# Kernel optimization log

Measured on AMD Instinct MI355X. Metric: run time of the kernel, lower is better.

## Reference

```python
import jax, jax.numpy as jnp
import numpy as np

TAU = 1.5
SCALE = 0.125
EPS = 1e-5
H = 8

@jax.custom_vjp
def spike(u):
    return (u >= 0.0).astype(u.dtype)

def _spike_fwd(u):
    return spike(u), u

def _spike_bwd(u, g):
    # ATan surrogate gradient, alpha=2 (spikingjelly default)
    return (g / (1.0 + (jnp.pi * u) ** 2),)

spike.defvjp(_spike_fwd, _spike_bwd)

def lif_ms(xt):
    # xt: (T, ...) multi-step LIF, decay_input=True, v_th=1, hard reset to 0, detach_reset
    def step(v, x):
        v = v + (x - v) / TAU
        s = spike(v - 1.0)
        v = v * (1.0 - jax.lax.stop_gradient(s))
        return v, s
    _, s = jax.lax.scan(step, jnp.zeros_like(xt[0]), xt)
    return s

def bn(x, g, b, m, var):
    # eval-mode BatchNorm1d over channel dim of (B, C, L)
    inv = g / jnp.sqrt(var + EPS)
    return (x - m[None, :, None]) * inv[None, :, None] + b[None, :, None]

def setup_inputs() -> dict:
    key = jax.random.key(0)
    ks = jax.random.split(key, 16)
    B, C, T, N = 8, 512, 4, 256
    w_scale = 1.0 / np.sqrt(C)
    inp = {
        'x': jax.random.normal(ks[0], (B, C, T, N), jnp.float32),
        'wq': jax.random.normal(ks[1], (C, C), jnp.float32) * w_scale,
        'wk': jax.random.normal(ks[2], (C, C), jnp.float32) * w_scale,
        'wv': jax.random.normal(ks[3], (C, C), jnp.float32) * w_scale,
        'wp': jax.random.normal(ks[4], (C, C), jnp.float32) * w_scale,
        'bp': jnp.zeros((C,), jnp.float32),
        'gq': jax.random.uniform(ks[5], (C,), jnp.float32, 0.5, 1.5),
        'bq': jax.random.uniform(ks[6], (C,), jnp.float32),
        'mq': jnp.zeros((C,), jnp.float32),
        'vq': jnp.ones((C,), jnp.float32),
        'gk': jax.random.uniform(ks[7], (C,), jnp.float32, 0.5, 1.5),
        'bk': jax.random.uniform(ks[8], (C,), jnp.float32),
        'mk': jnp.zeros((C,), jnp.float32),
        'vk': jnp.ones((C,), jnp.float32),
        'gv': jax.random.uniform(ks[9], (C,), jnp.float32, 0.5, 1.5),
        'bv': jax.random.uniform(ks[10], (C,), jnp.float32),
        'mv': jnp.zeros((C,), jnp.float32),
        'vv': jnp.ones((C,), jnp.float32),
        'gp': jax.random.uniform(ks[11], (C,), jnp.float32, 0.5, 1.5),
        'bpn': jax.random.uniform(ks[12], (C,), jnp.float32),
        'mp': jnp.zeros((C,), jnp.float32),
        'vp': jnp.ones((C,), jnp.float32),
    }
    return inp

def reference(x, wq, wk, wv, wp, bp, gq, bq, mq, vq, gk, bk, mk, vk,
              gv, bv, mv, vv, gp, bpn, mp, vp):
    B, C, T, N = x.shape
    L = T * N
    d = C // H

    # proj_bn then multi-step proj_lif over time dim
    xb = bn(x.reshape(B, C, L), gp, bpn, mp, vp).reshape(B, C, T, N)
    s0 = lif_ms(jnp.transpose(xb, (2, 0, 1, 3)))            # (T,B,C,N)
    x_for_qkv = jnp.transpose(s0, (1, 2, 0, 3)).reshape(B, C, L)  # (B,C,L)

    def qkv_branch(w, g, b_, m, v_):
        y = bn(jnp.einsum('oc,bcl->bol', w, x_for_qkv), g, b_, m, v_)
        y = y.reshape(B, C, T, N)
        sy = lif_ms(jnp.transpose(y, (2, 0, 1, 3)))         # (T,B,C,N)
        sy = jnp.transpose(sy, (1, 0, 3, 2)).reshape(B, L, C)  # (B,T,N,C)->(B,L,C)
        return jnp.transpose(sy.reshape(B, L, H, d), (0, 2, 1, 3))  # (B,H,L,d)

    q = qkv_branch(wq, gq, bq, mq, vq)
    k = qkv_branch(wk, gk, bk, mk, vk)
    v = qkv_branch(wv, gv, bv, mv, vv)

    attn = jnp.einsum('bhqd,bhkd->bhqk', q, k)              # no softmax
    o = jnp.einsum('bhqk,bhkd->bhqd', attn, v) * SCALE
    o = jnp.transpose(o, (0, 1, 3, 2)).reshape(B, C, L)

    # single-step attn_lif: v = o/tau from zero state, spike at threshold 1
    s = spike(o / TAU - 1.0)

    out = jnp.einsum('oc,bcl->bol', wp, s) + bp[None, :, None]
    return out.reshape(B, C, T, N)
```

## Files before the change

kernel.cpp:

```cpp
#include <hip/hip_runtime.h>
#include <hip/hip_bf16.h>


#define NB 8
#define NC 512
#define NT 4
#define NN 256
#define NL 1024
#define NH 8
#define ND 64
#define BCL (NB*NC*NL)

typedef __attribute__((ext_vector_type(8))) short  short8v;
typedef __attribute__((ext_vector_type(8))) unsigned short us8;
typedef __attribute__((ext_vector_type(4))) unsigned short us4;
typedef __attribute__((ext_vector_type(4))) float f32x4;

__device__ __forceinline__ float bu2f(unsigned short u) {
  return __uint_as_float(((unsigned)u) << 16);
}
__device__ __forceinline__ unsigned short f2bu(float f) {
  unsigned b = __float_as_uint(f);
  return (unsigned short)((b + 0x7FFFu + ((b >> 16) & 1u)) >> 16);
}

__global__ void k_prep(const float* __restrict__ wq, const float* __restrict__ wk,
                       const float* __restrict__ wv, const float* __restrict__ wp,
                       const float* __restrict__ x,
                       const float* __restrict__ g,  const float* __restrict__ bt,
                       const float* __restrict__ mu, const float* __restrict__ var,
                       unsigned short* __restrict__ H2,
                       unsigned short* __restrict__ ST0) {
  if (blockIdx.x < 512) {
    int gi = blockIdx.x * 256 + threadIdx.x;
    int p = gi >> 15;
    int o = (gi >> 6) & 511;
    int k8 = gi & 63;
    int rt = o >> 7, r = o & 127;
    int k0i = k8 >> 3, chunk = k8 & 7;
    const float* W = (p == 0) ? wq : (p == 1) ? wk : (p == 2) ? wv : wp;
    const float* src = W + (size_t)o * NC + k8 * 8;
    us8 a[3];
#pragma unroll
    for (int i = 0; i < 8; i++) {
      float w = src[i];
      unsigned short u1 = f2bu(w);
      float r1 = w - bu2f(u1);
      unsigned short u2 = f2bu(r1);
      float r2 = r1 - bu2f(u2);
      unsigned short u3 = f2bu(r2);
      a[0][i] = u1; a[1][i] = u2; a[2][i] = u3;
    }
#pragma unroll
    for (int j = 0; j < 3; j++) {
      size_t off = ((size_t)((((p * 3 + j) * 4 + rt) * 8 + k0i) * 8 + chunk)) * 1024
                   + (size_t)r * 8;
      *(us8*)&H2[off] = a[j];
    }
  } else {
    int bidx = blockIdx.x - 512;
    int b  = bidx >> 6;
    int c0 = (bidx & 63) * 8;
    int n  = threadIdx.x;
    unsigned short spk[NT][8];
#pragma unroll
    for (int i = 0; i < 8; i++) {
      int c = c0 + i;
      float inv = g[c] / sqrtf(var[c] + 1e-5f);
      float m = mu[c], be = bt[c];
      const float* xp = x + ((size_t)(b * NC + c)) * NL + n;
      float v = 0.f;
#pragma unroll
      for (int t = 0; t < NT; t++) {
        float y = (xp[t * NN] - m) * inv + be;
        v = v + (y - v) / 1.5f;
        unsigned short s = 0;
        if (v - 1.0f >= 0.f) { s = 0x3F80; v = 0.f; }
        spk[t][i] = s;
      }
    }
#pragma unroll
    for (int t = 0; t < NT; t++) {
      us8 pk;
#pragma unroll
      for (int i = 0; i < 8; i++) pk[i] = spk[t][i];
      *(us8*)&ST0[((size_t)b * NL + t * NN + n) * NC + c0] = pk;
    }
  }
}

__global__ __launch_bounds__(256) void
k_qkv(const unsigned short* __restrict__ H2,
      const unsigned short* __restrict__ ST0,
      const float* __restrict__ gq, const float* __restrict__ bq,
      const float* __restrict__ mq, const float* __restrict__ vq,
      const float* __restrict__ gk, const float* __restrict__ bk,
      const float* __restrict__ mk, const float* __restrict__ vk,
      const float* __restrict__ gv, const float* __restrict__ bv,
      const float* __restrict__ mv, const float* __restrict__ vv,
      unsigned short* __restrict__ STq, unsigned short* __restrict__ STk,
      unsigned short* __restrict__ STv) {
  __shared__ __align__(16) unsigned short sB[2][128 * 64];

  int id = blockIdx.x;
  int xcd = id & 7, slot = id >> 3;
  int qq = xcd * 96 + slot;
  int grp = qq >> 6, mi = qq & 63;
  int p = grp >> 2, rt = grp & 3;
  int b = mi >> 3;
  int n0 = (mi & 7) * 32;

  int tid = threadIdx.x;
  int w = tid >> 6, lane = tid & 63, quad = lane >> 4, l15 = lane & 15;
  int xorv = l15 & 7;

  const unsigned short* Sb = ST0 + (size_t)b * NL * NC;
  const unsigned short* Hbase = H2 + ((size_t)((p * 3) * 4 + rt) * 8) * 8192;

  f32x4 acc[2][8];
#pragma unroll
  for (int ri = 0; ri < 2; ri++)
#pragma unroll
    for (int jj = 0; jj < 8; jj++) acc[ri][jj] = (f32x4){0.f, 0.f, 0.f, 0.f};

  short8v A0[2][3][2], A1[2][3][2];

#define QLOADA(DST, K0I)                                                     \
  _Pragma("unroll") for (int ks = 0; ks < 2; ks++) {                         \
    int c8 = ks * 4 + quad;                                                  \
    _Pragma("unroll") for (int j = 0; j < 3; j++) {                          \
      const unsigned short* Hj =                                             \
          Hbase + ((size_t)(j * 4 * 8 + (K0I))) * 8192 + (size_t)c8 * 1024;  \
      DST[ks][j][0] = *(const short8v*)&Hj[(w * 32 + l15) * 8];              \
      DST[ks][j][1] = *(const short8v*)&Hj[(w * 32 + 16 + l15) * 8];         \
    }                                                                        \
  }

  QLOADA(A0, 0);

  us8 breg[4];
  int ccs[4], segs[4];
  size_t bsrc[4];
#pragma unroll
  for (int i = 0; i < 4; i++) {
    int idx = tid + i * 256;
    int cc = idx >> 3, seg = idx & 7;
    int t = (cc >> 4) & 3, nn = (cc & 15) | ((cc >> 6) << 4);
    ccs[i] = cc; segs[i] = seg;
    bsrc[i] = (size_t)(t * NN + n0 + nn) * NC + seg * 8;
  }
#pragma unroll
  for (int i = 0; i < 4; i++) breg[i] = *(const us8*)&Sb[bsrc[i]];
#pragma unroll
  for (int i = 0; i < 4; i++)
    *(us8*)&sB[0][ccs[i] * 64 + ((segs[i] ^ (ccs[i] & 7)) << 3)] = breg[i];

#define QBPRE(K0N)                                                           \
  _Pragma("unroll") for (int i = 0; i < 4; i++)                              \
    breg[i] = *(const us8*)&Sb[bsrc[i] + (size_t)(K0N) * 64];

#define QBWRITE(BUFN)                                                        \
  _Pragma("unroll") for (int i = 0; i < 4; i++)                              \
    *(us8*)&sB[BUFN][ccs[i] * 64 + ((segs[i] ^ (ccs[i] & 7)) << 3)] = breg[i];

#define QMFMAS(AR, BUF)                                                      \
  _Pragma("unroll") for (int ks = 0; ks < 2; ks++) {                         \
    int c8 = ks * 4 + quad;                                                  \
    int poff = (c8 ^ xorv) << 3;                                             \
    short8v bf[8];                                                           \
    _Pragma("unroll") for (int jj = 0; jj < 8; jj++)                         \
      bf[jj] = *(const short8v*)&sB[BUF][(jj * 16 + l15) * 64 + poff];       \
    _Pragma("unroll") for (int j = 0; j < 3; j++)                            \
      _Pragma("unroll") for (int jj = 0; jj < 8; jj++) {                     \
        acc[0][jj] = __builtin_amdgcn_mfma_f32_16x16x32_bf16(                \
            AR[ks][j][0], bf[jj], acc[0][jj], 0, 0, 0);                      \
        acc[1][jj] = __builtin_amdgcn_mfma_f32_16x16x32_bf16(                \
            AR[ks][j][1], bf[jj], acc[1][jj], 0, 0, 0);                      \
      }                                                                      \
  }

#define QSTEP(K0I, ACUR, ANXT)                                               \
  __syncthreads();                                                           \
  { if ((K0I) < 7) { QLOADA(ANXT, (K0I) + 1); } }                            \
  { if ((K0I) < 7) { QBPRE((K0I) + 1); } }                                   \
  QMFMAS(ACUR, (K0I) & 1);                                                   \
  { if ((K0I) < 7) { QBWRITE(((K0I) & 1) ^ 1); } }

  QSTEP(0, A0, A1)
  QSTEP(1, A1, A0)
  QSTEP(2, A0, A1)
  QSTEP(3, A1, A0)
  QSTEP(4, A0, A1)
  QSTEP(5, A1, A0)
  QSTEP(6, A0, A1)
  QSTEP(7, A1, A0)

#undef QLOADA
#undef QBPRE
#undef QBWRITE
#undef QMFMAS
#undef QSTEP

  const float *g, *bb, *mpt, *vr;
  unsigned short* So;
  if (p == 0)      { g = gq; bb = bq; mpt = mq; vr = vq; So = STq; }
  else if (p == 1) { g = gk; bb = bk; mpt = mk; vr = vk; So = STk; }
  else             { g = gv; bb = bv; mpt = mv; vr = vv; So = STv; }
  So += (size_t)b * NL * NC;

#pragma unroll
  for (int ri = 0; ri < 2; ri++) {
    int ob = rt * 128 + w * 32 + ri * 16 + quad * 4;
    float av[4], mvv[4], bvv[4];
#pragma unroll
    for (int r = 0; r < 4; r++) {
      av[r]  = g[ob + r] / sqrtf(vr[ob + r] + 1e-5f);
      mvv[r] = mpt[ob + r];
      bvv[r] = bb[ob + r];
    }
#pragma unroll
    for (int nh = 0; nh < 2; nh++) {
      int n = n0 + (nh << 4) + l15;
      unsigned short sp[4][4];
#pragma unroll
      for (int r = 0; r < 4; r++) {
        float vmem = 0.f;
#pragma unroll
        for (int t = 0; t < NT; t++) {
          float y = (acc[ri][nh * 4 + t][r] - mvv[r]) * av[r] + bvv[r];
          vmem = vmem + (y - vmem) / 1.5f;
          unsigned short s = 0;
          if (vmem - 1.0f >= 0.f) { s = 0x3F80; vmem = 0.f; }
          sp[t][r] = s;
        }
      }
#pragma unroll
      for (int t = 0; t < NT; t++) {
        us4 pk;
#pragma unroll
        for (int r = 0; r < 4; r++) pk[r] = sp[t][r];
        *(us4*)&So[(size_t)(t * NN + n) * NC + ob] = pk;
      }
    }
  }
}

__global__ void k_kvM(const unsigned short* __restrict__ STk,
                      const unsigned short* __restrict__ STv,
                      float* __restrict__ Mpart) {
  int bh = blockIdx.x, ch = blockIdx.y;
  int b = bh >> 3, h = bh & 7;
  const unsigned short* Kp = STk + (size_t)b * NL * NC + h * ND;
  const unsigned short* Vp = STv + (size_t)b * NL * NC + h * ND;
  __shared__ float sK[64][72];
  __shared__ float sV[64][72];
  int tid = threadIdx.x, tx = tid & 15, ty = tid >> 4;
  float acc[4][4] = {};
  for (int lt = 0; lt < 2; lt++) {
    int lb = ch * 128 + lt * 64;
#pragma unroll
    for (int i = 0; i < 2; i++) {
      int idx = tid + i * 256;
      int r = idx >> 3, seg = idx & 7;
      us8 kv = *(const us8*)&Kp[(size_t)(lb + r) * NC + seg * 8];
      us8 vv = *(const us8*)&Vp[(size_t)(lb + r) * NC + seg * 8];
#pragma unroll
      for (int q2 = 0; q2 < 8; q2++) {
        sK[r][seg * 8 + q2] = bu2f(kv[q2]);
        sV[r][seg * 8 + q2] = bu2f(vv[q2]);
      }
    }
    __syncthreads();
#pragma unroll 8
    for (int lc = 0; lc < 64; lc++) {
      float kvx[4], vvx[4];
#pragma unroll
      for (int i = 0; i < 4; i++) kvx[i] = sK[lc][ty * 4 + i];
#pragma unroll
      for (int j2 = 0; j2 < 4; j2++) vvx[j2] = sV[lc][tx * 4 + j2];
#pragma unroll
      for (int i = 0; i < 4; i++)
#pragma unroll
        for (int j2 = 0; j2 < 4; j2++)
          acc[i][j2] += kvx[i] * vvx[j2];
    }
    __syncthreads();
  }
  float* Mp = Mpart + ((size_t)ch * 64 + bh) * 4096;
#pragma unroll
  for (int i = 0; i < 4; i++) {
    float4 v4 = make_float4(acc[i][0], acc[i][1], acc[i][2], acc[i][3]);
    *(float4*)&Mp[(ty * 4 + i) * ND + tx * 4] = v4;
  }
}

__global__ __launch_bounds__(256) void
k_attn(const unsigned short* __restrict__ STq,
       const float* __restrict__ Mpart,
       unsigned short* __restrict__ STs) {
  __shared__ unsigned short MT1[64 * 64];
  __shared__ unsigned short MT2[64 * 64];
  int lt = blockIdx.x, bh = blockIdx.y;
  int b = bh >> 3, h = bh & 7;
  int tid = threadIdx.x;
  int w = tid >> 6, lane = tid & 63, quad = lane >> 4, l15 = lane & 15;

#pragma unroll
  for (int i = 0; i < 4; i++) {
    int idx4 = tid + i * 256;
    float4 s = ((const float4*)Mpart)[(size_t)bh * 1024 + idx4];
#pragma unroll
    for (int ch = 1; ch < 8; ch++) {
      float4 t = ((const float4*)Mpart)[((size_t)ch * 64 + bh) * 1024 + idx4];
      s.x += t.x; s.y += t.y; s.z += t.z; s.w += t.w;
    }
    int e = idx4 >> 4;
    int dd0 = (idx4 * 4) & 63;
    int chunk = e >> 3;
    float sv[4] = {s.x, s.y, s.z, s.w};
#pragma unroll
    for (int r = 0; r < 4; r++) {
      int dd = dd0 + r;
      unsigned short u1 = f2bu(sv[r]);
      unsigned short u2 = f2bu(sv[r] - bu2f(u1));
      int pos = dd * 64 + (((chunk ^ (dd & 7)) << 3) | (e & 7));
      MT1[pos] = u1;
      MT2[pos] = u2;
    }
  }
  __syncthreads();

  const unsigned short* Qp = STq + (size_t)b * NL * NC + h * ND;
  int lbase = lt * 256 + w * 64;

  f32x4 acc[4][4];
#pragma unroll
  for (int dt = 0; dt < 4; dt++)
#pragma unroll
    for (int j = 0; j < 4; j++) acc[dt][j] = (f32x4){0.f, 0.f, 0.f, 0.f};

#pragma unroll
  for (int ks = 0; ks < 2; ks++) {
    short8v bq[4];
#pragma unroll
    for (int ltile = 0; ltile < 4; ltile++)
      bq[ltile] = *(const short8v*)&Qp[(size_t)(lbase + ltile * 16 + l15) * NC
                                       + ks * 32 + quad * 8];
    int c8 = ks * 4 + quad;
#pragma unroll
    for (int dt = 0; dt < 4; dt++) {
      int dd = dt * 16 + l15;
      int off = dd * 64 + ((c8 ^ (dd & 7)) << 3);
      short8v a1 = *(const short8v*)&MT1[off];
      short8v a2 = *(const short8v*)&MT2[off];
#pragma unroll
      for (int ltile = 0; ltile < 4; ltile++) {
        acc[dt][ltile] = __builtin_amdgcn_mfma_f32_16x16x32_bf16(a1, bq[ltile], acc[dt][ltile], 0, 0, 0);
        acc[dt][ltile] = __builtin_amdgcn_mfma_f32_16x16x32_bf16(a2, bq[ltile], acc[dt][ltile], 0, 0, 0);
      }
    }
  }

  unsigned short* Sp = STs + (size_t)b * NL * NC + h * ND;
#pragma unroll
  for (int dt = 0; dt < 4; dt++)
#pragma unroll
    for (int ltile = 0; ltile < 4; ltile++) {
      int l = lbase + ltile * 16 + l15;
      int dd = dt * 16 + quad * 4;
      us4 pk;
#pragma unroll
      for (int r = 0; r < 4; r++) pk[r] = (acc[dt][ltile][r] >= 12.0f) ? 0x3F80 : 0;
      *(us4*)&Sp[(size_t)l * NC + dd] = pk;
    }
}

__global__ __launch_bounds__(256) void
k_out(const unsigned short* __restrict__ H2,
      const unsigned short* __restrict__ STs,
      const float* __restrict__ bp, float* __restrict__ out) {
  __shared__ __align__(16) unsigned short sB[2][64 * 64];

  int id = blockIdx.x;
  int xcd = id & 7, slot = id >> 3;
  int qq = xcd * 64 + slot;
  int rt = qq >> 7;
  int mi = qq & 127;
  int b  = mi >> 4;
  int l0 = (mi & 15) * 64;

  int tid = threadIdx.x;
  int w = tid >> 6, lane = tid & 63, quad = lane >> 4, l15 = lane & 15;
  int xorv = l15 & 7;

  const unsigned short* Sb = STs + (size_t)b * NL * NC;
  const unsigned short* Hbase = H2 + ((size_t)(9 * 4 + rt) * 8) * 8192;

  f32x4 acc[2][4];
#pragma unroll
  for (int ri = 0; ri < 2; ri++)
#pragma unroll
    for (int jj = 0; jj < 4; jj++) acc[ri][jj] = (f32x4){0.f, 0.f, 0.f, 0.f};

  short8v A0[2][3][2], A1[2][3][2];

#define OLOADA(DST, K0I)                                                     \
  _Pragma("unroll") for (int ks = 0; ks < 2; ks++) {                         \
    int c8 = ks * 4 + quad;                                                  \
    _Pragma("unroll") for (int j = 0; j < 3; j++) {                          \
      const unsigned short* Hj =                                             \
          Hbase + ((size_t)(j * 4 * 8 + (K0I))) * 8192 + (size_t)c8 * 1024;  \
      DST[ks][j][0] = *(const short8v*)&Hj[(w * 32 + l15) * 8];              \
      DST[ks][j][1] = *(const short8v*)&Hj[(w * 32 + 16 + l15) * 8];         \
    }                                                                        \
  }

  OLOADA(A0, 0);

  us8 breg[2];
  int ccs[2], segs[2];
  size_t bsrc[2];
#pragma unroll
  for (int i = 0; i < 2; i++) {
    int idx = tid + i * 256;
    int cc = idx >> 3, seg = idx & 7;
    ccs[i] = cc; segs[i] = seg;
    bsrc[i] = (size_t)(l0 + cc) * NC + seg * 8;
  }
#pragma unroll
  for (int i = 0; i < 2; i++) breg[i] = *(const us8*)&Sb[bsrc[i]];
#pragma unroll
  for (int i = 0; i < 2; i++)
    *(us8*)&sB[0][ccs[i] * 64 + ((segs[i] ^ (ccs[i] & 7)) << 3)] = breg[i];

#define OBPRE(K0N)                                                           \
  _Pragma("unroll") for (int i = 0; i < 2; i++)                              \
    breg[i] = *(const us8*)&Sb[bsrc[i] + (size_t)(K0N) * 64];

#define OBWRITE(BUFN)                                                        \
  _Pragma("unroll") for (int i = 0; i < 2; i++)                              \
    *(us8*)&sB[BUFN][ccs[i] * 64 + ((segs[i] ^ (ccs[i] & 7)) << 3)] = breg[i];

#define OMFMAS(AR, BUF)                                                      \
  _Pragma("unroll") for (int ks = 0; ks < 2; ks++) {                         \
    int c8 = ks * 4 + quad;                                                  \
    int poff = (c8 ^ xorv) << 3;                                             \
    short8v bf[4];                                                           \
    _Pragma("unroll") for (int jj = 0; jj < 4; jj++)                         \
      bf[jj] = *(const short8v*)&sB[BUF][(jj * 16 + l15) * 64 + poff];       \
    _Pragma("unroll") for (int j = 0; j < 3; j++)                            \
      _Pragma("unroll") for (int jj = 0; jj < 4; jj++) {                     \
        acc[0][jj] = __builtin_amdgcn_mfma_f32_16x16x32_bf16(                \
            AR[ks][j][0], bf[jj], acc[0][jj], 0, 0, 0);                      \
        acc[1][jj] = __builtin_amdgcn_mfma_f32_16x16x32_bf16(                \
            AR[ks][j][1], bf[jj], acc[1][jj], 0, 0, 0);                      \
      }                                                                      \
  }

#define OSTEP(K0I, ACUR, ANXT)                                               \
  __syncthreads();                                                           \
  { if ((K0I) < 7) { OLOADA(ANXT, (K0I) + 1); } }                            \
  { if ((K0I) < 7) { OBPRE((K0I) + 1); } }                                   \
  OMFMAS(ACUR, (K0I) & 1);                                                   \
  { if ((K0I) < 7) { OBWRITE(((K0I) & 1) ^ 1); } }

  OSTEP(0, A0, A1)
  OSTEP(1, A1, A0)
  OSTEP(2, A0, A1)
  OSTEP(3, A1, A0)
  OSTEP(4, A0, A1)
  OSTEP(5, A1, A0)
  OSTEP(6, A0, A1)
  OSTEP(7, A1, A0)

#undef OLOADA
#undef OBPRE
#undef OBWRITE
#undef OMFMAS
#undef OSTEP

#pragma unroll
  for (int ri = 0; ri < 2; ri++) {
    int ob = rt * 128 + w * 32 + ri * 16 + quad * 4;
#pragma unroll
    for (int jj = 0; jj < 4; jj++) {
      int l = l0 + jj * 16 + l15;
#pragma unroll
      for (int r = 0; r < 4; r++)
        out[((size_t)(b * NC + ob + r)) * NL + l] = acc[ri][jj][r] + bp[ob + r];
    }
  }
}

extern "C" void kernel_launch(void* const* d_in, const int* in_sizes, int n_in,
                              void* d_out, int out_size, void* d_ws, size_t ws_size,
                              hipStream_t stream) {
  (void)in_sizes; (void)n_in; (void)out_size; (void)ws_size;
  const float* x   = (const float*)d_in[0];
  const float* wq  = (const float*)d_in[1];
  const float* wk  = (const float*)d_in[2];
  const float* wv  = (const float*)d_in[3];
  const float* wp  = (const float*)d_in[4];
  const float* bp  = (const float*)d_in[5];
  const float* gq  = (const float*)d_in[6];
  const float* bq  = (const float*)d_in[7];
  const float* mq  = (const float*)d_in[8];
  const float* vq  = (const float*)d_in[9];
  const float* gk  = (const float*)d_in[10];
  const float* bk  = (const float*)d_in[11];
  const float* mk  = (const float*)d_in[12];
  const float* vk  = (const float*)d_in[13];
  const float* gv  = (const float*)d_in[14];
  const float* bv  = (const float*)d_in[15];
  const float* mv  = (const float*)d_in[16];
  const float* vvv = (const float*)d_in[17];
  const float* gp  = (const float*)d_in[18];
  const float* bpn = (const float*)d_in[19];
  const float* mp  = (const float*)d_in[20];
  const float* vp  = (const float*)d_in[21];

  unsigned short* H2  = (unsigned short*)d_ws;
  unsigned short* ST0 = H2 + (size_t)4 * 3 * NC * NC;
  unsigned short* STq = ST0 + BCL;
  unsigned short* STk = STq + BCL;
  unsigned short* STv = STk + BCL;
  unsigned short* STs = STv + BCL;
  float* Mpart = (float*)(STs + BCL);

  dim3 blk(256);
  k_prep<<<1024, blk, 0, stream>>>(wq, wk, wv, wp, x, gp, bpn, mp, vp, H2, ST0);
  k_qkv<<<768, blk, 0, stream>>>(H2, ST0,
      gq, bq, mq, vq, gk, bk, mk, vk, gv, bv, mv, vvv, STq, STk, STv);
  k_kvM<<<dim3(64, 8), blk, 0, stream>>>(STk, STv, Mpart);
  k_attn<<<dim3(4, 64), blk, 0, stream>>>(STq, Mpart, STs);
  k_out<<<512, blk, 0, stream>>>(H2, STs, bp, (float*)d_out);
}
```

Baseline: 185.3 us.

## Stage B tiles with direct global-to-LDS loads using pre-swizzled spike layout

Replaces the register-staged global load plus swizzled LDS write with global_load_lds direct copies in both the QKV and output projection GEMMs. To keep the bank-conflict-avoiding XOR swizzle, the producers (k_prep and the attention kernel) now write spike tensors with the swizzle already applied in global memory. s_setprio raises wave priority around the MFMA block. This removes VGPR staging and the LDS store instructions, at the cost of a swizzled global layout and reliance on the barrier for completion of the async copies.

```diff
diff --git a/kernel.cpp b/kernel.cpp
--- a/kernel.cpp
+++ b/kernel.cpp
@@ -22,6 +22,11 @@
 __device__ __forceinline__ unsigned short f2bu(float f) {
   unsigned b = __float_as_uint(f);
   return (unsigned short)((b + 0x7FFFu + ((b >> 16) & 1u)) >> 16);
+}
+__device__ __forceinline__ void gl16(const void* g, void* l) {
+  __builtin_amdgcn_global_load_lds(
+      (const __attribute__((address_space(1))) unsigned int*)(g),
+      (__attribute__((address_space(3))) unsigned int*)(l), 16, 0, 0);
 }
 
 __global__ void k_prep(const float* __restrict__ wq, const float* __restrict__ wk,
@@ -60,8 +65,10 @@
   } else {
     int bidx = blockIdx.x - 512;
     int b  = bidx >> 6;
-    int c0 = (bidx & 63) * 8;
+    int j  = bidx & 63;
+    int c0 = j * 8;
     int n  = threadIdx.x;
+    int slot = j ^ (n & 7);
     unsigned short spk[NT][8];
 #pragma unroll
     for (int i = 0; i < 8; i++) {
@@ -84,7 +91,7 @@
       us8 pk;
 #pragma unroll
       for (int i = 0; i < 8; i++) pk[i] = spk[t][i];
-      *(us8*)&ST0[((size_t)b * NL + t * NN + n) * NC + c0] = pk;
+      *(us8*)&ST0[((size_t)b * NL + t * NN + n) * NC + slot * 8] = pk;
     }
   }
 }
@@ -136,32 +143,21 @@
     }                                                                        \
   }
 
-  QLOADA(A0, 0);
-
-  us8 breg[4];
-  int ccs[4], segs[4];
   size_t bsrc[4];
 #pragma unroll
   for (int i = 0; i < 4; i++) {
     int idx = tid + i * 256;
     int cc = idx >> 3, seg = idx & 7;
     int t = (cc >> 4) & 3, nn = (cc & 15) | ((cc >> 6) << 4);
-    ccs[i] = cc; segs[i] = seg;
     bsrc[i] = (size_t)(t * NN + n0 + nn) * NC + seg * 8;
   }
-#pragma unroll
-  for (int i = 0; i < 4; i++) breg[i] = *(const us8*)&Sb[bsrc[i]];
-#pragma unroll
-  for (int i = 0; i < 4; i++)
-    *(us8*)&sB[0][ccs[i] * 64 + ((segs[i] ^ (ccs[i] & 7)) << 3)] = breg[i];
-
-#define QBPRE(K0N)                                                           \
+
+#define QSTAGE(K0N, BUFN)                                                    \
   _Pragma("unroll") for (int i = 0; i < 4; i++)                              \
-    breg[i] = *(const us8*)&Sb[bsrc[i] + (size_t)(K0N) * 64];
-
-#define QBWRITE(BUFN)                                                        \
-  _Pragma("unroll") for (int i = 0; i < 4; i++)                              \
-    *(us8*)&sB[BUFN][ccs[i] * 64 + ((segs[i] ^ (ccs[i] & 7)) << 3)] = breg[i];
+    gl16(&Sb[bsrc[i] + (size_t)(K0N) * 64], &sB[BUFN][(tid + i * 256) * 8]);
+
+  QSTAGE(0, 0);
+  QLOADA(A0, 0);
 
 #define QMFMAS(AR, BUF)                                                      \
   _Pragma("unroll") for (int ks = 0; ks < 2; ks++) {                         \
@@ -182,9 +178,10 @@
 #define QSTEP(K0I, ACUR, ANXT)                                               \
   __syncthreads();                                                           \
   { if ((K0I) < 7) { QLOADA(ANXT, (K0I) + 1); } }                            \
-  { if ((K0I) < 7) { QBPRE((K0I) + 1); } }                                   \
+  { if ((K0I) < 7) { QSTAGE((K0I) + 1, ((K0I) & 1) ^ 1); } }                 \
+  __builtin_amdgcn_s_setprio(1);                                             \
   QMFMAS(ACUR, (K0I) & 1);                                                   \
-  { if ((K0I) < 7) { QBWRITE(((K0I) & 1) ^ 1); } }
+  __builtin_amdgcn_s_setprio(0);
 
   QSTEP(0, A0, A1)
   QSTEP(1, A1, A0)
@@ -196,8 +193,7 @@
   QSTEP(7, A1, A0)
 
 #undef QLOADA
-#undef QBPRE
-#undef QBWRITE
+#undef QSTAGE
 #undef QMFMAS
 #undef QSTEP
 
@@ -361,17 +357,20 @@
     }
   }
 
-  unsigned short* Sp = STs + (size_t)b * NL * NC + h * ND;
+  unsigned short* Sp = STs + (size_t)b * NL * NC;
 #pragma unroll
   for (int dt = 0; dt < 4; dt++)
 #pragma unroll
     for (int ltile = 0; ltile < 4; ltile++) {
       int l = lbase + ltile * 16 + l15;
-      int dd = dt * 16 + quad * 4;
+      int colshort = h * ND + dt * 16 + quad * 4;
+      int chunk = colshort >> 3;
+      int half  = colshort & 7;
+      int slt = chunk ^ (l & 7);
       us4 pk;
 #pragma unroll
       for (int r = 0; r < 4; r++) pk[r] = (acc[dt][ltile][r] >= 12.0f) ? 0x3F80 : 0;
-      *(us4*)&Sp[(size_t)l * NC + dd] = pk;
+      *(us4*)&Sp[(size_t)l * NC + (slt << 3) + half] = pk;
     }
 }
 
@@ -415,31 +414,19 @@
     }                                                                        \
   }
 
-  OLOADA(A0, 0);
-
-  us8 breg[2];
-  int ccs[2], segs[2];
   size_t bsrc[2];
 #pragma unroll
   for (int i = 0; i < 2; i++) {
     int idx = tid + i * 256;
-    int cc = idx >> 3, seg = idx & 7;
-    ccs[i] = cc; segs[i] = seg;
-    bsrc[i] = (size_t)(l0 + cc) * NC + seg * 8;
-  }
-#pragma unroll
-  for (int i = 0; i < 2; i++) breg[i] = *(const us8*)&Sb[bsrc[i]];
-#pragma unroll
-  for (int i = 0; i < 2; i++)
-    *(us8*)&sB[0][ccs[i] * 64 + ((segs[i] ^ (ccs[i] & 7)) << 3)] = breg[i];
-
-#define OBPRE(K0N)                                                           \
+    bsrc[i] = (size_t)(l0 + (idx >> 3)) * NC + (idx & 7) * 8;
+  }
+
+#define OSTAGE(K0N, BUFN)                                                    \
   _Pragma("unroll") for (int i = 0; i < 2; i++)                              \
-    breg[i] = *(const us8*)&Sb[bsrc[i] + (size_t)(K0N) * 64];
-
-#define OBWRITE(BUFN)                                                        \
-  _Pragma("unroll") for (int i = 0; i < 2; i++)                              \
-    *(us8*)&sB[BUFN][ccs[i] * 64 + ((segs[i] ^ (ccs[i] & 7)) << 3)] = breg[i];
+    gl16(&Sb[bsrc[i] + (size_t)(K0N) * 64], &sB[BUFN][(tid + i * 256) * 8]);
+
+  OSTAGE(0, 0);
+  OLOADA(A0, 0);
 
 #define OMFMAS(AR, BUF)                                                      \
   _Pragma("unroll") for (int ks = 0; ks < 2; ks++) {                         \
@@ -460,9 +447,10 @@
 #define OSTEP(K0I, ACUR, ANXT)                                               \
   __syncthreads();                                                           \
   { if ((K0I) < 7) { OLOADA(ANXT, (K0I) + 1); } }                            \
-  { if ((K0I) < 7) { OBPRE((K0I) + 1); } }                                   \
+  { if ((K0I) < 7) { OSTAGE((K0I) + 1, ((K0I) & 1) ^ 1); } }                 \
+  __builtin_amdgcn_s_setprio(1);                                             \
   OMFMAS(ACUR, (K0I) & 1);                                                   \
-  { if ((K0I) < 7) { OBWRITE(((K0I) & 1) ^ 1); } }
+  __builtin_amdgcn_s_setprio(0);
 
   OSTEP(0, A0, A1)
   OSTEP(1, A1, A0)
@@ -474,8 +462,7 @@
   OSTEP(7, A1, A0)
 
 #undef OLOADA
-#undef OBPRE
-#undef OBWRITE
+#undef OSTAGE
 #undef OMFMAS
 #undef OSTEP
 
```

After: 190.1 us. 2.5% more time.

## Store K/V spikes transposed and compute K^T V with bf16 MFMA

Applied to the files above, without the earlier changes.

The QKV kernel now writes the K and V spike tensors in a channel-major (C, L) layout, so the K^T·V reduction can load contiguous sequence runs directly as MFMA operands. k_kvM replaces its fp32 shared-memory outer-product loop with 16x16x32 bf16 MFMA instructions that read straight from global memory. This is meant to remove the FP32 FMA cost and the LDS staging. In exchange, the epilogue for K and V now does scalar 2-byte stores strided by NL, which may coalesce poorly and slow k_qkv.

```diff
diff --git a/kernel.cpp b/kernel.cpp
--- a/kernel.cpp
+++ b/kernel.cpp
@@ -98,8 +98,8 @@
       const float* __restrict__ mk, const float* __restrict__ vk,
       const float* __restrict__ gv, const float* __restrict__ bv,
       const float* __restrict__ mv, const float* __restrict__ vv,
-      unsigned short* __restrict__ STq, unsigned short* __restrict__ STk,
-      unsigned short* __restrict__ STv) {
+      unsigned short* __restrict__ STq, unsigned short* __restrict__ STkT,
+      unsigned short* __restrict__ STvT) {
   __shared__ __align__(16) unsigned short sB[2][128 * 64];
 
   int id = blockIdx.x;
@@ -204,8 +204,8 @@
   const float *g, *bb, *mpt, *vr;
   unsigned short* So;
   if (p == 0)      { g = gq; bb = bq; mpt = mq; vr = vq; So = STq; }
-  else if (p == 1) { g = gk; bb = bk; mpt = mk; vr = vk; So = STk; }
-  else             { g = gv; bb = bv; mpt = mv; vr = vv; So = STv; }
+  else if (p == 1) { g = gk; bb = bk; mpt = mk; vr = vk; So = STkT; }
+  else             { g = gv; bb = bv; mpt = mv; vr = vv; So = STvT; }
   So += (size_t)b * NL * NC;
 
 #pragma unroll
@@ -234,64 +234,58 @@
           sp[t][r] = s;
         }
       }
-#pragma unroll
-      for (int t = 0; t < NT; t++) {
-        us4 pk;
-#pragma unroll
-        for (int r = 0; r < 4; r++) pk[r] = sp[t][r];
-        *(us4*)&So[(size_t)(t * NN + n) * NC + ob] = pk;
+      if (p == 0) {
+#pragma unroll
+        for (int t = 0; t < NT; t++) {
+          us4 pk;
+#pragma unroll
+          for (int r = 0; r < 4; r++) pk[r] = sp[t][r];
+          *(us4*)&So[(size_t)(t * NN + n) * NC + ob] = pk;
+        }
+      } else {
+#pragma unroll
+        for (int t = 0; t < NT; t++)
+#pragma unroll
+          for (int r = 0; r < 4; r++)
+            So[(size_t)(ob + r) * NL + t * NN + n] = sp[t][r];
       }
     }
   }
 }
 
-__global__ void k_kvM(const unsigned short* __restrict__ STk,
-                      const unsigned short* __restrict__ STv,
-                      float* __restrict__ Mpart) {
+__global__ __launch_bounds__(256) void
+k_kvM(const unsigned short* __restrict__ STkT,
+      const unsigned short* __restrict__ STvT,
+      float* __restrict__ Mpart) {
   int bh = blockIdx.x, ch = blockIdx.y;
   int b = bh >> 3, h = bh & 7;
-  const unsigned short* Kp = STk + (size_t)b * NL * NC + h * ND;
-  const unsigned short* Vp = STv + (size_t)b * NL * NC + h * ND;
-  __shared__ float sK[64][72];
-  __shared__ float sV[64][72];
-  int tid = threadIdx.x, tx = tid & 15, ty = tid >> 4;
-  float acc[4][4] = {};
-  for (int lt = 0; lt < 2; lt++) {
-    int lb = ch * 128 + lt * 64;
-#pragma unroll
-    for (int i = 0; i < 2; i++) {
-      int idx = tid + i * 256;
-      int r = idx >> 3, seg = idx & 7;
-      us8 kv = *(const us8*)&Kp[(size_t)(lb + r) * NC + seg * 8];
-      us8 vv = *(const us8*)&Vp[(size_t)(lb + r) * NC + seg * 8];
-#pragma unroll
-      for (int q2 = 0; q2 < 8; q2++) {
-        sK[r][seg * 8 + q2] = bu2f(kv[q2]);
-        sV[r][seg * 8 + q2] = bu2f(vv[q2]);
-      }
-    }
-    __syncthreads();
-#pragma unroll 8
-    for (int lc = 0; lc < 64; lc++) {
-      float kvx[4], vvx[4];
-#pragma unroll
-      for (int i = 0; i < 4; i++) kvx[i] = sK[lc][ty * 4 + i];
-#pragma unroll
-      for (int j2 = 0; j2 < 4; j2++) vvx[j2] = sV[lc][tx * 4 + j2];
-#pragma unroll
-      for (int i = 0; i < 4; i++)
-#pragma unroll
-        for (int j2 = 0; j2 < 4; j2++)
-          acc[i][j2] += kvx[i] * vvx[j2];
-    }
-    __syncthreads();
-  }
+  const unsigned short* KT = STkT + ((size_t)(b * NC + h * ND)) * NL;
+  const unsigned short* VT = STvT + ((size_t)(b * NC + h * ND)) * NL;
+  int tid = threadIdx.x;
+  int w = tid >> 6, lane = tid & 63, quad = lane >> 4, l15 = lane & 15;
+  int lb = ch * 128;
+
+  f32x4 acc[4];
+#pragma unroll
+  for (int jj = 0; jj < 4; jj++) acc[jj] = (f32x4){0.f, 0.f, 0.f, 0.f};
+
+#pragma unroll
+  for (int ks = 0; ks < 4; ks++) {
+    int lc = lb + ks * 32 + quad * 8;
+    short8v a = *(const short8v*)&KT[(size_t)(w * 16 + l15) * NL + lc];
+#pragma unroll
+    for (int jj = 0; jj < 4; jj++) {
+      short8v bv = *(const short8v*)&VT[(size_t)(jj * 16 + l15) * NL + lc];
+      acc[jj] = __builtin_amdgcn_mfma_f32_16x16x32_bf16(a, bv, acc[jj], 0, 0, 0);
+    }
+  }
+
   float* Mp = Mpart + ((size_t)ch * 64 + bh) * 4096;
 #pragma unroll
-  for (int i = 0; i < 4; i++) {
-    float4 v4 = make_float4(acc[i][0], acc[i][1], acc[i][2], acc[i][3]);
-    *(float4*)&Mp[(ty * 4 + i) * ND + tx * 4] = v4;
-  }
+  for (int jj = 0; jj < 4; jj++)
+#pragma unroll
+    for (int r = 0; r < 4; r++)
+      Mp[(w * 16 + quad * 4 + r) * ND + jj * 16 + l15] = acc[jj][r];
 }
 
 __global__ __launch_bounds__(256) void
@@ -519,19 +513,19 @@
   const float* mp  = (const float*)d_in[20];
   const float* vp  = (const float*)d_in[21];
 
-  unsigned short* H2  = (unsigned short*)d_ws;
-  unsigned short* ST0 = H2 + (size_t)4 * 3 * NC * NC;
-  unsigned short* STq = ST0 + BCL;
-  unsigned short* STk = STq + BCL;
-  unsigned short* STv = STk + BCL;
-  unsigned short* STs = STv + BCL;
+  unsigned short* H2   = (unsigned short*)d_ws;
+  unsigned short* ST0  = H2 + (size_t)4 * 3 * NC * NC;
+  unsigned short* STq  = ST0 + BCL;
+  unsigned short* STkT = STq + BCL;
+  unsigned short* STvT = STkT + BCL;
+  unsigned short* STs  = STvT + BCL;
   float* Mpart = (float*)(STs + BCL);
 
   dim3 blk(256);
   k_prep<<<1024, blk, 0, stream>>>(wq, wk, wv, wp, x, gp, bpn, mp, vp, H2, ST0);
   k_qkv<<<768, blk, 0, stream>>>(H2, ST0,
-      gq, bq, mq, vq, gk, bk, mk, vk, gv, bv, mv, vvv, STq, STk, STv);
-  k_kvM<<<dim3(64, 8), blk, 0, stream>>>(STk, STv, Mpart);
+      gq, bq, mq, vq, gk, bk, mk, vk, gv, bv, mv, vvv, STq, STkT, STvT);
+  k_kvM<<<dim3(64, 8), blk, 0, stream>>>(STkT, STvT, Mpart);
   k_attn<<<dim3(4, 64), blk, 0, stream>>>(STq, Mpart, STs);
   k_out<<<512, blk, 0, stream>>>(H2, STs, bp, (float*)d_out);
 }
```

New measurement: 184.9 us. Within noise of the previous version (-0.2%).
